# Kernel tuning notes

Measured on AMD Instinct MI355X. Metric: run time of the kernel, lower is better.

The kernel has to match this reference:

```python
import jax, jax.numpy as jnp
import numpy as np

EMBED_DIM = 1024
NUM_HEADS = 16
HEAD_DIM = EMBED_DIM // NUM_HEADS


def setup_inputs() -> dict:
    key = jax.random.key(0)
    ks = jax.random.split(key, 9)
    B, S, D = 1, 4096, EMBED_DIM
    scale = 1.0 / np.sqrt(D)
    x = jax.random.normal(ks[0], (B, S, D), dtype=jnp.float32)
    # Linear weights stored as [in, out]; torch nn.Linear init ~ U(-1/sqrt(in), 1/sqrt(in))
    wq = jax.random.uniform(ks[1], (D, D), jnp.float32, -scale, scale)
    bq = jax.random.uniform(ks[2], (D,), jnp.float32, -scale, scale)
    wk = jax.random.uniform(ks[3], (D, D), jnp.float32, -scale, scale)
    bk = jax.random.uniform(ks[4], (D,), jnp.float32, -scale, scale)
    wv = jax.random.uniform(ks[5], (D, D), jnp.float32, -scale, scale)
    bv = jax.random.uniform(ks[6], (D,), jnp.float32, -scale, scale)
    wo = jax.random.uniform(ks[7], (D, D), jnp.float32, -scale, scale)
    bo = jax.random.uniform(ks[8], (D,), jnp.float32, -scale, scale)
    return {"x": x, "wq": wq, "bq": bq, "wk": wk, "bk": bk,
            "wv": wv, "bv": bv, "wo": wo, "bo": bo}


def reference(x, wq, bq, wk, bk, wv, bv, wo, bo):
    B, S, D = x.shape
    H, Hd = NUM_HEADS, HEAD_DIM
    # QKV projections
    q = x @ wq + bq  # [B,S,D]
    k = x @ wk + bk
    v = x @ wv + bv
    # split heads -> [B,H,S,Hd]
    q = q.reshape(B, S, H, Hd).transpose(0, 2, 1, 3)
    k = k.reshape(B, S, H, Hd).transpose(0, 2, 1, 3)
    v = v.reshape(B, S, H, Hd).transpose(0, 2, 1, 3)
    inv_sqrt_d = 1.0 / np.sqrt(Hd).astype(np.float32)
    scores = jnp.einsum('bhqd,bhkd->bhqk', q, k) * inv_sqrt_d  # [B,H,S,S]
    attn = jax.nn.softmax(scores, axis=-1)
    out = jnp.einsum('bhqk,bhkd->bhqd', attn, v)  # [B,H,S,Hd]
    out = out.transpose(0, 2, 1, 3).reshape(B, S, D)
    return out @ wo + bo
```

## Files before the change

kernel.cpp:

```cpp
#include <hip/hip_runtime.h>

typedef unsigned short u16;
typedef unsigned int u32;
typedef short v8s __attribute__((ext_vector_type(8)));
typedef float f32x4 __attribute__((ext_vector_type(4)));
typedef float f32x16 __attribute__((ext_vector_type(16)));

#define S_LEN 4096
#define DM 1024
#define HDIM 64
#define CEXP 0.18033688f

__device__ __forceinline__ u16 f2bs(float f) {
  u32 u = __float_as_uint(f);
  u32 r = 0x7FFFu + ((u >> 16) & 1u);
  return (u16)((u + r) >> 16);
}

__device__ __forceinline__ float fexp2(float x) {
  float r;
  asm("v_exp_f32 %0, %1" : "=v"(r) : "v"(x));
  return r;
}

__device__ __forceinline__ void gstage16(const void* g, void* lds_wave_base) {
  __builtin_amdgcn_global_load_lds(
      (const __attribute__((address_space(1))) u32*)g,
      (__attribute__((address_space(3))) u32*)lds_wave_base, 16, 0, 0);
}

__device__ __forceinline__ f32x16 vzero16() {
  f32x16 v;
#pragma unroll
  for (int r = 0; r < 16; ++r) v[r] = 0.f;
  return v;
}

__global__ __launch_bounds__(256) void k_prep(
    const float* __restrict__ x,
    const float* __restrict__ w0, const float* __restrict__ w1,
    const float* __restrict__ w2, const float* __restrict__ w3,
    u16* __restrict__ xb,
    u16* __restrict__ t0, u16* __restrict__ t1,
    u16* __restrict__ t2, u16* __restrict__ t3) {
  const int z = blockIdx.z;
  if (z < 4) {
    __shared__ float tile[32][33];
    const float* w; u16* wt;
    switch (z) {
      case 0: w = w0; wt = t0; break;
      case 1: w = w1; wt = t1; break;
      case 2: w = w2; wt = t2; break;
      default: w = w3; wt = t3; break;
    }
    const int r = threadIdx.x >> 3;
    const int c4 = (threadIdx.x & 7) * 4;
    const int k0 = blockIdx.x * 32, n0 = blockIdx.y * 32;
    float4 v = *reinterpret_cast<const float4*>(w + (size_t)(k0 + r) * DM + n0 + c4);
    tile[r][c4] = v.x; tile[r][c4 + 1] = v.y; tile[r][c4 + 2] = v.z; tile[r][c4 + 3] = v.w;
    __syncthreads();
    u16 o4[4] = {f2bs(tile[c4][r]), f2bs(tile[c4 + 1][r]),
                 f2bs(tile[c4 + 2][r]), f2bs(tile[c4 + 3][r])};
    *reinterpret_cast<uint2*>(wt + (size_t)(n0 + r) * DM + k0 + c4) =
        *reinterpret_cast<const uint2*>(o4);
  } else {
    const int ci = ((z - 4) * 1024 + blockIdx.y * 32 + blockIdx.x) * 256 + threadIdx.x;
    const float4* p = reinterpret_cast<const float4*>(x) + (size_t)ci * 2;
    float4 a = p[0], b = p[1];
    u16 t[8] = {f2bs(a.x), f2bs(a.y), f2bs(a.z), f2bs(a.w),
                f2bs(b.x), f2bs(b.y), f2bs(b.z), f2bs(b.w)};
    reinterpret_cast<uint4*>(xb)[ci] = *reinterpret_cast<const uint4*>(t);
  }
}

template <int MODE>
__device__ __forceinline__ void gemm_core(
    u16* __restrict__ As, u16* __restrict__ Bs,
    const u16* __restrict__ A, const u16* __restrict__ Bt,
    const float* __restrict__ bias, void* __restrict__ Cout, float oscale) {
  constexpr int K = DM;
  const int tid = threadIdx.x;
  const int lane = tid & 63, wave = tid >> 6;
  const int wm = wave >> 1, wn = wave & 1;
  const int l15 = lane & 15, l4 = lane >> 4;
  const int bm0 = blockIdx.x * 128, bn0 = blockIdx.y * 128;

  f32x4 acc[4][4];
#pragma unroll
  for (int m = 0; m < 4; ++m)
#pragma unroll
    for (int n = 0; n < 4; ++n) acc[m][n] = 0.f;

  const int s0 = tid, s1 = tid + 256;
  const int ra0 = s0 >> 2, ca0 = ((s0 & 3) ^ ((ra0 >> 1) & 3)) * 8;
  const int ra1 = s1 >> 2, ca1 = ((s1 & 3) ^ ((ra1 >> 1) & 3)) * 8;
  const u16* Ab = A + (size_t)bm0 * K;
  const u16* Bb = Bt + (size_t)bn0 * K;
  u16* ldsA0 = As + (size_t)(wave * 64) * 8;
  u16* ldsA1 = As + (size_t)(256 + wave * 64) * 8;
  u16* ldsB0 = Bs + (size_t)(wave * 64) * 8;
  u16* ldsB1 = Bs + (size_t)(256 + wave * 64) * 8;

  for (int k0 = 0; k0 < K; k0 += 32) {
    gstage16(Ab + (size_t)ra0 * K + k0 + ca0, ldsA0);
    gstage16(Ab + (size_t)ra1 * K + k0 + ca1, ldsA1);
    gstage16(Bb + (size_t)ra0 * K + k0 + ca0, ldsB0);
    gstage16(Bb + (size_t)ra1 * K + k0 + ca1, ldsB1);
    __syncthreads();
    v8s af[4], bfr[4];
#pragma unroll
    for (int m = 0; m < 4; ++m) {
      const int rowa = wm * 64 + m * 16 + l15;
      af[m] = *reinterpret_cast<const v8s*>(
          As + (size_t)(rowa * 4 + (l4 ^ ((rowa >> 1) & 3))) * 8);
      const int rowb = wn * 64 + m * 16 + l15;
      bfr[m] = *reinterpret_cast<const v8s*>(
          Bs + (size_t)(rowb * 4 + (l4 ^ ((rowb >> 1) & 3))) * 8);
    }
#pragma unroll
    for (int m = 0; m < 4; ++m)
#pragma unroll
      for (int n = 0; n < 4; ++n)
        acc[m][n] = __builtin_amdgcn_mfma_f32_16x16x32_bf16(af[m], bfr[n], acc[m][n], 0, 0, 0);
    __syncthreads();
  }

#pragma unroll
  for (int m = 0; m < 4; ++m) {
    const int gs0 = bm0 + wm * 64 + m * 16 + l4 * 4;
#pragma unroll
    for (int n = 0; n < 4; ++n) {
      const int gn = bn0 + wn * 64 + n * 16 + l15;
      const float bv = bias[gn];
      if (MODE == 0) {
        u16* O = (u16*)Cout;
        const size_t base = (size_t)(gn >> 6) * (S_LEN * HDIM) + (size_t)(gn & 63);
#pragma unroll
        for (int r = 0; r < 4; ++r)
          O[base + (size_t)(gs0 + r) * HDIM] = f2bs((acc[m][n][r] + bv) * oscale);
      } else {
        u16* O = (u16*)Cout;
        u16 p4[4];
#pragma unroll
        for (int r = 0; r < 4; ++r) p4[r] = f2bs(acc[m][n][r] + bv);
        *reinterpret_cast<uint2*>(O + (size_t)(gn >> 6) * (HDIM * S_LEN) +
                                  (size_t)(gn & 63) * S_LEN + gs0) =
            *reinterpret_cast<const uint2*>(p4);
      }
    }
  }
}

__global__ __launch_bounds__(256) void k_gemm_qkv(
    const u16* __restrict__ A,
    const u16* __restrict__ wq, const u16* __restrict__ wk, const u16* __restrict__ wv,
    const float* __restrict__ bq, const float* __restrict__ bk, const float* __restrict__ bv,
    u16* __restrict__ Qo, u16* __restrict__ Ko, u16* __restrict__ Vo) {
  __shared__ __attribute__((aligned(16))) u16 As[128 * 32];
  __shared__ __attribute__((aligned(16))) u16 Bs[128 * 32];
  const int z = blockIdx.z;
  if (z == 0)      gemm_core<0>(As, Bs, A, wq, bq, Qo, CEXP);
  else if (z == 1) gemm_core<0>(As, Bs, A, wk, bk, Ko, 1.f);
  else             gemm_core<1>(As, Bs, A, wv, bv, Vo, 1.f);
}

__global__ __launch_bounds__(256) void k_gemm_o(
    const u16* __restrict__ A, const u16* __restrict__ wo,
    const float* __restrict__ bo, float* __restrict__ out) {
  __shared__ __attribute__((aligned(16))) u16 As[128 * 32];
  __shared__ __attribute__((aligned(16))) u16 Bs[64 * 32];
  constexpr int K = DM, N = DM;
  const int tid = threadIdx.x;
  const int lane = tid & 63, wave = tid >> 6;
  const int wm = wave >> 1, wn = wave & 1;
  const int l15 = lane & 15, l4 = lane >> 4;
  const int bm0 = blockIdx.x * 128, bn0 = blockIdx.y * 64;

  f32x4 acc[4][2];
#pragma unroll
  for (int m = 0; m < 4; ++m)
#pragma unroll
    for (int n = 0; n < 2; ++n) acc[m][n] = 0.f;

  const int s0 = tid, s1 = tid + 256;
  const int ra0 = s0 >> 2, ca0 = ((s0 & 3) ^ ((ra0 >> 1) & 3)) * 8;
  const int ra1 = s1 >> 2, ca1 = ((s1 & 3) ^ ((ra1 >> 1) & 3)) * 8;
  const int rb = tid >> 2,  cb = ((tid & 3) ^ ((rb >> 1) & 3)) * 8;
  const u16* Ab = A + (size_t)bm0 * K;
  const u16* Bb = wo + (size_t)bn0 * K;
  u16* ldsA0 = As + (size_t)(wave * 64) * 8;
  u16* ldsA1 = As + (size_t)(256 + wave * 64) * 8;
  u16* ldsB0 = Bs + (size_t)(wave * 64) * 8;

  for (int k0 = 0; k0 < K; k0 += 32) {
    gstage16(Ab + (size_t)ra0 * K + k0 + ca0, ldsA0);
    gstage16(Ab + (size_t)ra1 * K + k0 + ca1, ldsA1);
    gstage16(Bb + (size_t)rb * K + k0 + cb, ldsB0);
    __syncthreads();
    v8s af[4], bfr[2];
#pragma unroll
    for (int m = 0; m < 4; ++m) {
      const int rowa = wm * 64 + m * 16 + l15;
      af[m] = *reinterpret_cast<const v8s*>(
          As + (size_t)(rowa * 4 + (l4 ^ ((rowa >> 1) & 3))) * 8);
    }
#pragma unroll
    for (int n = 0; n < 2; ++n) {
      const int rowb = wn * 32 + n * 16 + l15;
      bfr[n] = *reinterpret_cast<const v8s*>(
          Bs + (size_t)(rowb * 4 + (l4 ^ ((rowb >> 1) & 3))) * 8);
    }
#pragma unroll
    for (int m = 0; m < 4; ++m)
#pragma unroll
      for (int n = 0; n < 2; ++n)
        acc[m][n] = __builtin_amdgcn_mfma_f32_16x16x32_bf16(af[m], bfr[n], acc[m][n], 0, 0, 0);
    __syncthreads();
  }

#pragma unroll
  for (int m = 0; m < 4; ++m) {
    const int gs0 = bm0 + wm * 64 + m * 16 + l4 * 4;
#pragma unroll
    for (int n = 0; n < 2; ++n) {
      const int gn = bn0 + wn * 32 + n * 16 + l15;
      const float bv = bo[gn];
#pragma unroll
      for (int r = 0; r < 4; ++r)
        out[(size_t)(gs0 + r) * N + gn] = acc[m][n][r] + bv;
    }
  }
}

__global__ __launch_bounds__(256, 2) void k_attn(
    const u16* __restrict__ Q, const u16* __restrict__ Kg,
    const u16* __restrict__ Vt, u16* __restrict__ Aout) {
  __shared__ __attribute__((aligned(16))) u16 Ks[4][64 * 64];
  __shared__ __attribute__((aligned(16))) u16 Vs[4][64 * 64];

  const int tid = threadIdx.x;
  const int lane = tid & 63, wave = tid >> 6;
  const int l31 = lane & 31, lh = lane >> 5;

  const int id = blockIdx.x;
  const int xcd = id & 7, sp = id >> 3;
  const int h = xcd * 2 + (sp & 1);
  const int qb = sp >> 1;
  const int q0 = qb * 128 + wave * 32;

  const u16* Qh = Q + (size_t)h * S_LEN * HDIM;
  const u16* Kh = Kg + (size_t)h * S_LEN * HDIM;
  const u16* Vh = Vt + (size_t)h * HDIM * S_LEN;

  v8s qf[4];
#pragma unroll
  for (int ks = 0; ks < 4; ++ks)
    qf[ks] = *reinterpret_cast<const v8s*>(
        Qh + (size_t)(q0 + l31) * HDIM + ks * 16 + lh * 8);

  const f32x16 z16 = vzero16();
  f32x16 oacc[2];
  oacc[0] = z16; oacc[1] = z16;
  float lsum = 0.f;

  const int s0i = tid, s1i = tid + 256;
  const int r0 = s0i >> 3, c0 = ((s0i & 7) ^ (r0 & 7)) * 8;
  const int r1 = s1i >> 3, c1 = ((s1i & 7) ^ (r1 & 7)) * 8;

  auto stageKV = [&](int b, int t) {
    const int kv0 = t * 64;
    gstage16(Kh + (size_t)(kv0 + r0) * HDIM + c0, &Ks[b][(wave * 64) * 8]);
    gstage16(Kh + (size_t)(kv0 + r1) * HDIM + c1, &Ks[b][(256 + wave * 64) * 8]);
    gstage16(Vh + (size_t)r0 * S_LEN + kv0 + c0, &Vs[b][(wave * 64) * 8]);
    gstage16(Vh + (size_t)r1 * S_LEN + kv0 + c1, &Vs[b][(256 + wave * 64) * 8]);
  };

  auto qk = [&](const u16* Kb, f32x16 (&sO)[2]) {
    __builtin_amdgcn_s_setprio(1);
#pragma unroll
    for (int j = 0; j < 2; ++j) {
      const int row = j * 32 + l31;
      v8s k0 = *reinterpret_cast<const v8s*>(
          Kb + (size_t)(row * 8 + ((0 + lh) ^ (row & 7))) * 8);
      sO[j] = __builtin_amdgcn_mfma_f32_32x32x16_bf16(k0, qf[0], z16, 0, 0, 0);
#pragma unroll
      for (int ks = 1; ks < 4; ++ks) {
        v8s kf = *reinterpret_cast<const v8s*>(
            Kb + (size_t)(row * 8 + ((ks * 2 + lh) ^ (row & 7))) * 8);
        sO[j] = __builtin_amdgcn_mfma_f32_32x32x16_bf16(kf, qf[ks], sO[j], 0, 0, 0);
      }
    }
    __builtin_amdgcn_s_setprio(0);
  };

  auto halfTile = [&](const u16* Vb, f32x16 (&sIn)[2]) {
    v8s vf[2][4];
#pragma unroll
    for (int n = 0; n < 2; ++n) {
      const int row = n * 32 + l31;
#pragma unroll
      for (int ks = 0; ks < 4; ++ks)
        vf[n][ks] = *reinterpret_cast<const v8s*>(
            Vb + (size_t)(row * 8 + ((ks * 2 + lh) ^ (row & 7))) * 8);
    }

    v8s pf[4];
#pragma unroll
    for (int jj = 0; jj < 2; ++jj) {
      float p[16];
#pragma unroll
      for (int r = 0; r < 16; ++r) p[r] = fexp2(sIn[jj][r]);
      lsum += ((p[0] + p[1]) + (p[2] + p[3])) + ((p[4] + p[5]) + (p[6] + p[7])) +
              (((p[8] + p[9]) + (p[10] + p[11])) + ((p[12] + p[13]) + (p[14] + p[15])));
      u32 X1, X2, X3, X4, Y1, Y2, Y3, Y4;
      asm("v_cvt_pk_bf16_f32 %0, %1, %2" : "=v"(X1) : "v"(p[0]), "v"(p[1]));
      asm("v_cvt_pk_bf16_f32 %0, %1, %2" : "=v"(Y1) : "v"(p[4]), "v"(p[5]));
      asm("v_cvt_pk_bf16_f32 %0, %1, %2" : "=v"(X2) : "v"(p[2]), "v"(p[3]));
      asm("v_cvt_pk_bf16_f32 %0, %1, %2" : "=v"(Y2) : "v"(p[6]), "v"(p[7]));
      asm("v_cvt_pk_bf16_f32 %0, %1, %2" : "=v"(X3) : "v"(p[8]), "v"(p[9]));
      asm("v_cvt_pk_bf16_f32 %0, %1, %2" : "=v"(Y3) : "v"(p[12]), "v"(p[13]));
      asm("v_cvt_pk_bf16_f32 %0, %1, %2" : "=v"(X4) : "v"(p[10]), "v"(p[11]));
      asm("v_cvt_pk_bf16_f32 %0, %1, %2" : "=v"(Y4) : "v"(p[14]), "v"(p[15]));
      asm("v_permlane32_swap_b32 %0, %1" : "+v"(X1), "+v"(Y1));
      asm("v_permlane32_swap_b32 %0, %1" : "+v"(X2), "+v"(Y2));
      asm("v_permlane32_swap_b32 %0, %1" : "+v"(X3), "+v"(Y3));
      asm("v_permlane32_swap_b32 %0, %1" : "+v"(X4), "+v"(Y4));
      uint4 w0; w0.x = X1; w0.y = X2; w0.z = Y1; w0.w = Y2;
      uint4 w1; w1.x = X3; w1.y = X4; w1.z = Y3; w1.w = Y4;
      pf[jj * 2 + 0] = *reinterpret_cast<const v8s*>(&w0);
      pf[jj * 2 + 1] = *reinterpret_cast<const v8s*>(&w1);
    }

    __builtin_amdgcn_s_setprio(1);
#pragma unroll
    for (int ks = 0; ks < 4; ++ks) {
      oacc[0] = __builtin_amdgcn_mfma_f32_32x32x16_bf16(pf[ks], vf[0][ks], oacc[0], 0, 0, 0);
      oacc[1] = __builtin_amdgcn_mfma_f32_32x32x16_bf16(pf[ks], vf[1][ks], oacc[1], 0, 0, 0);
    }
    __builtin_amdgcn_s_setprio(0);
  };

  f32x16 sacc0[2], sacc1[2];

  auto body2 = [&](int t, int b0, int b1, int b2, int b3, bool doStage) {
    asm volatile("s_waitcnt vmcnt(0)\n\ts_barrier" ::: "memory");
    if (doStage) { stageKV(b2, t + 2); stageKV(b3, t + 3); }
    qk(&Ks[b0][0], sacc0);
    qk(&Ks[b1][0], sacc1);
    halfTile(&Vs[b0][0], sacc0);
    halfTile(&Vs[b1][0], sacc1);
  };

  stageKV(0, 0);
  stageKV(1, 1);

  for (int tt = 0; tt < 60; tt += 4) {
    body2(tt, 0, 1, 2, 3, true);
    body2(tt + 2, 2, 3, 0, 1, true);
  }
  body2(60, 0, 1, 2, 3, true);
  body2(62, 2, 3, 0, 1, false);

  u32 ua = __float_as_uint(lsum), ub = ua;
  asm("v_permlane32_swap_b32 %0, %1" : "+v"(ua), "+v"(ub));
  const float lf = __uint_as_float(ua) + __uint_as_float(ub);

#pragma unroll
  for (int r = 0; r < 16; ++r) {
    const int crow = (r & 3) + 8 * (r >> 2) + 4 * lh;
    const float inv = __builtin_amdgcn_rcpf(__shfl(lf, crow));
    const int q = q0 + crow;
    const size_t base = (size_t)q * DM + h * HDIM + l31;
    Aout[base] = f2bs(oacc[0][r] * inv);
    Aout[base + 32] = f2bs(oacc[1][r] * inv);
  }
}

extern "C" void kernel_launch(void* const* d_in, const int* in_sizes, int n_in,
                              void* d_out, int out_size, void* d_ws, size_t ws_size,
                              hipStream_t stream) {
  const float* x  = (const float*)d_in[0];
  const float* wq = (const float*)d_in[1];
  const float* bq = (const float*)d_in[2];
  const float* wk = (const float*)d_in[3];
  const float* bk = (const float*)d_in[4];
  const float* wv = (const float*)d_in[5];
  const float* bv = (const float*)d_in[6];
  const float* wo = (const float*)d_in[7];
  const float* bo = (const float*)d_in[8];
  float* out = (float*)d_out;

  char* ws = (char*)d_ws;
  u16* xb  = (u16*)(ws);
  u16* wqT = (u16*)(ws + (8u << 20));
  u16* wkT = wqT + 1024 * 1024;
  u16* wvT = wkT + 1024 * 1024;
  u16* woT = wvT + 1024 * 1024;
  u16* Qh  = (u16*)(ws + (16u << 20));
  u16* Kh  = Qh + 16 * 4096 * 64;
  u16* Vth = Kh + 16 * 4096 * 64;
  u16* Ao  = Vth + 16 * 4096 * 64;

  dim3 pg(32, 32, 6);
  k_prep<<<pg, 256, 0, stream>>>(x, wq, wk, wv, wo, xb, wqT, wkT, wvT, woT);
  dim3 gg(32, 8, 3);
  k_gemm_qkv<<<gg, 256, 0, stream>>>(xb, wqT, wkT, wvT, bq, bk, bv, Qh, Kh, Vth);
  k_attn<<<512, 256, 0, stream>>>(Qh, Kh, Vth, Ao);
  dim3 og(32, 16);
  k_gemm_o<<<og, 256, 0, stream>>>(Ao, woT, bo, out);
}
```

Baseline: 153.3 us.

## Double QKV GEMM K-step to 64 and reorder attention exp/pack before PV

The QKV projection GEMM now stages 64-wide K slices per barrier pair instead of 32, with an 8-chunk XOR swizzle, and doubles the shared-memory tiles. This halves the number of barrier round-trips in the K loop at the cost of more LDS per block, which may lower occupancy. In the attention loop, the exp/bf16 pack for both score tiles now runs before either PV matmul, so the VALU work can overlap with the MFMAs, at some cost in register pressure.

Result: no change. 151.7 us (-1.0%).

```diff
diff --git a/kernel.cpp b/kernel.cpp
--- a/kernel.cpp
+++ b/kernel.cpp
@@ -91,37 +91,41 @@
 #pragma unroll
     for (int n = 0; n < 4; ++n) acc[m][n] = 0.f;
 
-  const int s0 = tid, s1 = tid + 256;
-  const int ra0 = s0 >> 2, ca0 = ((s0 & 3) ^ ((ra0 >> 1) & 3)) * 8;
-  const int ra1 = s1 >> 2, ca1 = ((s1 & 3) ^ ((ra1 >> 1) & 3)) * 8;
+  int ra[4], ca[4];
+#pragma unroll
+  for (int i = 0; i < 4; ++i) {
+    const int s = i * 256 + tid;
+    ra[i] = s >> 3;
+    ca[i] = ((s & 7) ^ (ra[i] & 7)) * 8;
+  }
   const u16* Ab = A + (size_t)bm0 * K;
   const u16* Bb = Bt + (size_t)bn0 * K;
-  u16* ldsA0 = As + (size_t)(wave * 64) * 8;
-  u16* ldsA1 = As + (size_t)(256 + wave * 64) * 8;
-  u16* ldsB0 = Bs + (size_t)(wave * 64) * 8;
-  u16* ldsB1 = Bs + (size_t)(256 + wave * 64) * 8;
-
-  for (int k0 = 0; k0 < K; k0 += 32) {
-    gstage16(Ab + (size_t)ra0 * K + k0 + ca0, ldsA0);
-    gstage16(Ab + (size_t)ra1 * K + k0 + ca1, ldsA1);
-    gstage16(Bb + (size_t)ra0 * K + k0 + ca0, ldsB0);
-    gstage16(Bb + (size_t)ra1 * K + k0 + ca1, ldsB1);
+
+  for (int k0 = 0; k0 < K; k0 += 64) {
+#pragma unroll
+    for (int i = 0; i < 4; ++i) {
+      gstage16(Ab + (size_t)ra[i] * K + k0 + ca[i], As + (size_t)(i * 256 + wave * 64) * 8);
+      gstage16(Bb + (size_t)ra[i] * K + k0 + ca[i], Bs + (size_t)(i * 256 + wave * 64) * 8);
+    }
     __syncthreads();
-    v8s af[4], bfr[4];
-#pragma unroll
-    for (int m = 0; m < 4; ++m) {
-      const int rowa = wm * 64 + m * 16 + l15;
-      af[m] = *reinterpret_cast<const v8s*>(
-          As + (size_t)(rowa * 4 + (l4 ^ ((rowa >> 1) & 3))) * 8);
-      const int rowb = wn * 64 + m * 16 + l15;
-      bfr[m] = *reinterpret_cast<const v8s*>(
-          Bs + (size_t)(rowb * 4 + (l4 ^ ((rowb >> 1) & 3))) * 8);
-    }
-#pragma unroll
-    for (int m = 0; m < 4; ++m)
-#pragma unroll
-      for (int n = 0; n < 4; ++n)
-        acc[m][n] = __builtin_amdgcn_mfma_f32_16x16x32_bf16(af[m], bfr[n], acc[m][n], 0, 0, 0);
+#pragma unroll
+    for (int s = 0; s < 2; ++s) {
+      v8s af[4], bfr[4];
+#pragma unroll
+      for (int m = 0; m < 4; ++m) {
+        const int rowa = wm * 64 + m * 16 + l15;
+        af[m] = *reinterpret_cast<const v8s*>(
+            As + (size_t)(rowa * 8 + ((s * 4 + l4) ^ (rowa & 7))) * 8);
+        const int rowb = wn * 64 + m * 16 + l15;
+        bfr[m] = *reinterpret_cast<const v8s*>(
+            Bs + (size_t)(rowb * 8 + ((s * 4 + l4) ^ (rowb & 7))) * 8);
+      }
+#pragma unroll
+      for (int m = 0; m < 4; ++m)
+#pragma unroll
+        for (int n = 0; n < 4; ++n)
+          acc[m][n] = __builtin_amdgcn_mfma_f32_16x16x32_bf16(af[m], bfr[n], acc[m][n], 0, 0, 0);
+    }
     __syncthreads();
   }
 
@@ -156,8 +160,8 @@
     const u16* __restrict__ wq, const u16* __restrict__ wk, const u16* __restrict__ wv,
     const float* __restrict__ bq, const float* __restrict__ bk, const float* __restrict__ bv,
     u16* __restrict__ Qo, u16* __restrict__ Ko, u16* __restrict__ Vo) {
-  __shared__ __attribute__((aligned(16))) u16 As[128 * 32];
-  __shared__ __attribute__((aligned(16))) u16 Bs[128 * 32];
+  __shared__ __attribute__((aligned(16))) u16 As[128 * 64];
+  __shared__ __attribute__((aligned(16))) u16 Bs[128 * 64];
   const int z = blockIdx.z;
   if (z == 0)      gemm_core<0>(As, Bs, A, wq, bq, Qo, CEXP);
   else if (z == 1) gemm_core<0>(As, Bs, A, wk, bk, Ko, 1.f);
@@ -293,18 +297,7 @@
     __builtin_amdgcn_s_setprio(0);
   };
 
-  auto halfTile = [&](const u16* Vb, f32x16 (&sIn)[2]) {
-    v8s vf[2][4];
-#pragma unroll
-    for (int n = 0; n < 2; ++n) {
-      const int row = n * 32 + l31;
-#pragma unroll
-      for (int ks = 0; ks < 4; ++ks)
-        vf[n][ks] = *reinterpret_cast<const v8s*>(
-            Vb + (size_t)(row * 8 + ((ks * 2 + lh) ^ (row & 7))) * 8);
-    }
-
-    v8s pf[4];
+  auto pack = [&](f32x16 (&sIn)[2], v8s (&pf)[4]) {
 #pragma unroll
     for (int jj = 0; jj < 2; ++jj) {
       float p[16];
@@ -330,7 +323,18 @@
       pf[jj * 2 + 0] = *reinterpret_cast<const v8s*>(&w0);
       pf[jj * 2 + 1] = *reinterpret_cast<const v8s*>(&w1);
     }
-
+  };
+
+  auto pv = [&](const u16* Vb, v8s (&pf)[4]) {
+    v8s vf[2][4];
+#pragma unroll
+    for (int n = 0; n < 2; ++n) {
+      const int row = n * 32 + l31;
+#pragma unroll
+      for (int ks = 0; ks < 4; ++ks)
+        vf[n][ks] = *reinterpret_cast<const v8s*>(
+            Vb + (size_t)(row * 8 + ((ks * 2 + lh) ^ (row & 7))) * 8);
+    }
     __builtin_amdgcn_s_setprio(1);
 #pragma unroll
     for (int ks = 0; ks < 4; ++ks) {
@@ -347,8 +351,11 @@
     if (doStage) { stageKV(b2, t + 2); stageKV(b3, t + 3); }
     qk(&Ks[b0][0], sacc0);
     qk(&Ks[b1][0], sacc1);
-    halfTile(&Vs[b0][0], sacc0);
-    halfTile(&Vs[b1][0], sacc1);
+    v8s pf0[4], pf1[4];
+    pack(sacc0, pf0);
+    pack(sacc1, pf1);
+    pv(&Vs[b0][0], pf0);
+    pv(&Vs[b1][0], pf1);
   };
 
   stageKV(0, 0);
```
